# Performance work log

Hardware: AMD Instinct MI355X
Metric: run time of the kernel (lower is better)

Reference implementation:

```python
import jax, jax.numpy as jnp
import numpy as np

N_HEAD = 16
D_HEAD = 64
D_MODEL = 1024  # d_qry = d_key = d_val
D_HIDDEN = N_HEAD * D_HEAD


def setup_inputs() -> dict:
    key = jax.random.key(0)
    ks = jax.random.split(key, 9)
    b, n = 2, 2048
    s = 0.02
    return {
        "qry": jax.random.normal(ks[0], (b, n, D_MODEL), jnp.float32),
        "key": jax.random.normal(ks[1], (b, n, D_MODEL), jnp.float32),
        "val": jax.random.normal(ks[2], (b, n, D_MODEL), jnp.float32),
        "mask": jax.random.randint(ks[3], (b, n), 0, 2) > 0,  # key-side padding mask
        "Wq": jax.random.normal(ks[4], (D_MODEL, D_HIDDEN), jnp.float32) * s,
        "Wk": jax.random.normal(ks[5], (D_MODEL, D_HIDDEN), jnp.float32) * s,
        "Wv": jax.random.normal(ks[6], (D_MODEL, D_HIDDEN), jnp.float32) * s,
        "Wo": jax.random.normal(ks[7], (D_HIDDEN, D_MODEL), jnp.float32) * s,
        "bo": jax.random.normal(ks[8], (D_MODEL,), jnp.float32) * s,
    }


def reference(qry, key, val, mask, Wq, Wk, Wv, Wo, bo):
    b, n, _ = qry.shape
    scale = D_HEAD ** 0.5
    # projections, split into heads: [b, h, n, d]
    q = (qry @ Wq).reshape(b, n, N_HEAD, D_HEAD).transpose(0, 2, 1, 3)
    k = (key @ Wk).reshape(b, n, N_HEAD, D_HEAD).transpose(0, 2, 1, 3)
    v = (val @ Wv).reshape(b, n, N_HEAD, D_HEAD).transpose(0, 2, 1, 3)
    sim = jnp.einsum('bhid,bhjd->bhij', q, k) / scale  # full O(n^2) scores
    # key-side padding mask broadcast over heads and query positions
    sim = jnp.where(mask[:, None, None, :], sim, jnp.float32(-1e32))
    attn = jax.nn.softmax(sim, axis=-1)
    # NOTE: original applies dropout to `sim` after computing attn (a no-op on
    # the output); dropout=0.0 regardless, so attention weights are `attn`.
    x = jnp.einsum('bhij,bhjd->bhid', attn, v)
    x = x.transpose(0, 2, 1, 3).reshape(b, n, D_HIDDEN)
    return x @ Wo + bo
```

## Files before the change

### kernel.cpp

```cpp
#include <hip/hip_runtime.h>
#include <hip/hip_bf16.h>

using u16 = unsigned short;
using u32 = unsigned int;
using short8 = __attribute__((ext_vector_type(8))) short;
using f32x4  = __attribute__((ext_vector_type(4))) float;
using u32x4  = __attribute__((ext_vector_type(4))) u32;
using u32x2  = __attribute__((ext_vector_type(2))) u32;

union V16 { u32x4 u; short8 s; };

__device__ __forceinline__ u16 f2b(float f) {
  u32 u = __float_as_uint(f);
  u32 r = (u + 0x7FFFu + ((u >> 16) & 1u)) >> 16;
  return (u16)r;
}
__device__ __forceinline__ u32 pk2(u16 a, u16 b) {
  return (u32)a | ((u32)b << 16);
}
__device__ __forceinline__ u32 cvtpk(float lo, float hi) {
  u32 r;
  asm("v_cvt_pk_bf16_f32 %0, %1, %2" : "=v"(r) : "v"(lo), "v"(hi));
  return r;
}
__device__ __forceinline__ float ex2(float x) {
  float r;
  asm("v_exp_f32 %0, %1" : "=v"(r) : "v"(x));
  return r;
}
__device__ __forceinline__ void gld16(const u16* g, u16* l) {
  __builtin_amdgcn_global_load_lds(
      (const __attribute__((address_space(1))) u32*)g,
      (__attribute__((address_space(3))) u32*)l, 16, 0, 0);
}

#define KSCALE 0.18033688011f
#define SMAX   12.0f


__global__ __launch_bounds__(256) void wconv(
    const float* __restrict__ Wq, const float* __restrict__ Wk,
    const float* __restrict__ Wv, const float* __restrict__ Wo,
    u16* __restrict__ Wt, u16* __restrict__ WoT)
{
  __shared__ u16 T[64][130];
  const int zz = blockIdx.z;
  const float* src = (zz == 0) ? Wq : (zz == 1) ? Wk : (zz == 2) ? Wv : Wo;
  u16* dst = (zz < 3) ? (Wt + (size_t)zz * 1048576) : WoT;
  const int nt = blockIdx.x, ks = blockIdx.y;
  const int tid = threadIdx.x;

  {
    const int kl = tid >> 2, nl0 = (tid & 3) * 32;
    const float* sp = src + (size_t)(ks * 64 + kl) * 1024 + nt * 128 + nl0;
#pragma unroll
    for (int i = 0; i < 8; ++i) {
      f32x4 x = *(const f32x4*)(sp + i * 4);
      T[kl][nl0 + i * 4 + 0] = f2b(x[0]);
      T[kl][nl0 + i * 4 + 1] = f2b(x[1]);
      T[kl][nl0 + i * 4 + 2] = f2b(x[2]);
      T[kl][nl0 + i * 4 + 3] = f2b(x[3]);
    }
  }
  __syncthreads();

  const int c = tid >> 4, l0 = (tid & 15) * 4;
  u16* dp = dst + ((size_t)(nt * 16 + ks) * 16 + c) * 512 + l0 * 8;
#pragma unroll
  for (int dl = 0; dl < 4; ++dl) {
    const int l = l0 + dl;
    const int kl = (c & 1) * 32 + (l >> 4) * 8;
    const int nl = (c >> 3) * 64 + ((c >> 1) & 3) * 16 + (l & 15);
    u32x4 u;
#pragma unroll
    for (int p = 0; p < 4; ++p)
      u[p] = pk2(T[kl + 2 * p][nl], T[kl + 2 * p + 1][nl]);
    *(u32x4*)(dp + dl * 8) = u;
  }
}

__global__ __launch_bounds__(256) void maskscan(
    const int* __restrict__ mask, int* __restrict__ inv,
    float* __restrict__ cbias, int* __restrict__ ntb,
    u16* __restrict__ Kimg, u16* __restrict__ Vimg)
{
  const int h = blockIdx.x, b = blockIdx.y;
  const int tid = threadIdx.x;
  __shared__ int ssum[256];

  int m8[8], s = 0;
#pragma unroll
  for (int i = 0; i < 8; ++i) {
    m8[i] = mask[b * 2048 + tid * 8 + i] ? 1 : 0;
    s += m8[i];
  }
  ssum[tid] = s;
  __syncthreads();
  for (int off = 1; off < 256; off <<= 1) {
    int v = (tid >= off) ? ssum[tid - off] : 0;
    __syncthreads();
    ssum[tid] += v;
    __syncthreads();
  }
  const int nvalid = ssum[255];
  int run = ssum[tid] - s;

  if (h == 0) {
    int run2 = run;
#pragma unroll
    for (int i = 0; i < 8; ++i) {
      if (m8[i]) { inv[b * 2048 + run2] = tid * 8 + i; ++run2; }
    }
#pragma unroll
    for (int i = 0; i < 8; ++i) {
      const int idx = tid * 8 + i;
      cbias[b * 2048 + idx] = (idx < nvalid) ? -SMAX : -1e30f;
    }
    if (tid == 0) { ntb[b] = (nvalid + 63) >> 6; ntb[2 + b] = nvalid; }
  }

  const int pend = ((nvalid + 63) >> 6) << 6;
  for (int p = nvalid + tid; p < pend; p += 256) {
    const int kt2 = p >> 6, r = p & 63;
    const size_t base = ((size_t)((b * 16 + h) * 32 + kt2)) * 4096;
    const int t2 = ((r >> 5) << 1) | ((r >> 2) & 1);
    const int ll2 = (((r >> 3) & 3) << 2) | (r & 3);
#pragma unroll
    for (int s2 = 0; s2 < 2; ++s2)
#pragma unroll
      for (int lgk = 0; lgk < 4; ++lgk)
#pragma unroll
        for (int e = 0; e < 8; ++e)
          Kimg[base + (t2 * 2 + s2) * 512 + (lgk * 16 + ll2) * 8 + e] = 0;
    const int sv = r >> 5, lgv = (r >> 3) & 3, e0 = r & 7;
#pragma unroll
    for (int td = 0; td < 4; ++td)
#pragma unroll
      for (int llv = 0; llv < 16; ++llv)
        Vimg[base + (sv * 4 + td) * 512 + (lgv * 16 + llv) * 8 + e0] = 0;
  }
}

__global__ __launch_bounds__(256) void aconv(
    const float* __restrict__ Aq, const float* __restrict__ Ak,
    const float* __restrict__ Av, u16* __restrict__ Af,
    const int* __restrict__ inv, const int* __restrict__ ntbv,
    int z0, size_t zstride)
{
  const int z = blockIdx.z + z0;
  const float* A = (z == 0) ? Aq : (z == 1) ? Ak : Av;
  u16* dst = Af + (size_t)blockIdx.z * zstride;
  const int ks = blockIdx.x, mt = blockIdx.y;
  const int tid = threadIdx.x;
  const int r = tid >> 1, h = tid & 1;

  int srow = mt * 128 + r;
  if (z >= 1) {
    const int b = srow >> 11, cpos = srow & 2047;
    if (cpos >= ntbv[2 + b]) return;
    srow = b * 2048 + inv[b * 2048 + cpos];
  }

  const f32x4* sp = (const f32x4*)(A + (size_t)srow * 1024 + ks * 64 + h * 32);
  const int c = ((r >> 6) << 3) | (((r >> 4) & 3) << 1) | h;
  u16* dp = dst + ((size_t)(mt * 16 + ks) * 16 + c) * 512 + (r & 15) * 8;

#pragma unroll
  for (int lg = 0; lg < 4; ++lg) {
    f32x4 x0 = sp[2 * lg], x1 = sp[2 * lg + 1];
    u32x4 u;
    u[0] = cvtpk(x0[0], x0[1]); u[1] = cvtpk(x0[2], x0[3]);
    u[2] = cvtpk(x1[0], x1[1]); u[3] = cvtpk(x1[2], x1[3]);
    *(u32x4*)(dp + lg * 128) = u;
  }
}

__global__ __launch_bounds__(512, 4) void gemm_qkv_k(
    const u16* __restrict__ Af, const u16* __restrict__ Wt,
    u16* __restrict__ Qw, u16* __restrict__ Kw, u16* __restrict__ Vw,
    const int* __restrict__ ntbv, int z0, size_t azs)
{
  __shared__ u16 As[2][8192];
  __shared__ u16 Bs[2][8192];

  const int L = blockIdx.x;
  const int xcd = L & 7, idx = L >> 3;
  const int zi = idx >> 5;
  const int z = z0 + zi;
  const int mt = (z == 0) ? ((xcd << 2) | (idx & 3))
                          : (((idx & 3) << 3) | xcd);
  const int nt = (idx >> 2) & 7;

  if (z >= 1) {
    const int b0 = (mt * 128) >> 11;
    if ((mt * 128 & 2047) >= ntbv[2 + b0]) return;
  }

  const u16* Aimg = Af + (size_t)zi * azs;
  const u16* Bimg = Wt + (size_t)z * 1048576;
  u16* O = (z == 0) ? Qw : (z == 1) ? Kw : Vw;

  const int tid = threadIdx.x;
  const int w = tid >> 6, l = tid & 63, lg = l >> 4, ll = l & 15;
  const int wr = w >> 2, wc = w & 3;
  const size_t ab = (size_t)mt * 131072;
  const size_t bb = (size_t)nt * 131072;

  f32x4 acc[4][2];
#pragma unroll
  for (int i = 0; i < 4; ++i)
#pragma unroll
    for (int t = 0; t < 2; ++t)
      acc[i][t] = (f32x4){0.f, 0.f, 0.f, 0.f};

#define QKV_ISSUE(ksx, buf) do {                                           \
    const size_t ao_ = ab + (size_t)(ksx) * 8192;                          \
    const size_t bo_ = bb + (size_t)(ksx) * 8192;                          \
    gld16(Aimg + ao_ + (size_t)w * 512 + l * 8,       &As[buf][w * 512]);  \
    gld16(Aimg + ao_ + (size_t)(w + 8) * 512 + l * 8, &As[buf][(w + 8) * 512]); \
    gld16(Bimg + bo_ + (size_t)w * 512 + l * 8,       &Bs[buf][w * 512]);  \
    gld16(Bimg + bo_ + (size_t)(w + 8) * 512 + l * 8, &Bs[buf][(w + 8) * 512]); \
  } while (0)

  QKV_ISSUE(0, 0);

  for (int ks = 0; ks < 16; ++ks) {
    const int cur = ks & 1;
    asm volatile("s_waitcnt vmcnt(0)" ::: "memory");
    __builtin_amdgcn_sched_barrier(0);
    __builtin_amdgcn_s_barrier();
    __builtin_amdgcn_sched_barrier(0);

    if (ks + 1 < 16) QKV_ISSUE(ks + 1, cur ^ 1);

    short8 afr[2][4], bfr[2][2];
#pragma unroll
    for (int kk = 0; kk < 2; ++kk) {
#pragma unroll
      for (int i = 0; i < 4; ++i) {
        V16 v; v.u = *(const u32x4*)&As[cur][(wr * 8 + i * 2 + kk) * 512 + l * 8];
        afr[kk][i] = v.s;
      }
#pragma unroll
      for (int t = 0; t < 2; ++t) {
        V16 v; v.u = *(const u32x4*)&Bs[cur][((wc >> 1) * 8 + ((wc & 1) * 2 + t) * 2 + kk) * 512 + l * 8];
        bfr[kk][t] = v.s;
      }
    }
#pragma unroll
    for (int kk = 0; kk < 2; ++kk)
#pragma unroll
      for (int i = 0; i < 4; ++i)
#pragma unroll
        for (int t = 0; t < 2; ++t)
          acc[i][t] = __builtin_amdgcn_mfma_f32_16x16x32_bf16(afr[kk][i], bfr[kk][t], acc[i][t], 0, 0, 0);
  }
#undef QKV_ISSUE

  const int m0 = mt * 128, n0 = nt * 128;
  if (z == 0) {
#pragma unroll
    for (int i = 0; i < 4; ++i)
#pragma unroll
      for (int t = 0; t < 2; ++t) {
        const int n = n0 + wc * 32 + t * 16 + ll;
        const int h = n >> 6, dd = n & 63;
#pragma unroll
        for (int j = 0; j < 4; ++j) {
          const int m = m0 + wr * 64 + i * 16 + lg * 4 + j;
          const int bbk = m >> 11, pos = m & 2047;
          O[((size_t)(bbk * 16 + h) * 2048 + pos) * 64 + dd] = f2b(acc[i][t][j]);
        }
      }
  } else if (z == 1) {
    const int bbk = m0 >> 11;
    const int nv = ntbv[2 + bbk];
#pragma unroll
    for (int i = 0; i < 4; ++i)
#pragma unroll
      for (int t = 0; t < 2; ++t) {
        const int n = n0 + wc * 32 + t * 16 + ll;
        const int h = n >> 6, dd = n & 63;
        const int s = dd >> 5, lgk = (dd >> 3) & 3, e = dd & 7;
#pragma unroll
        for (int j = 0; j < 4; ++j) {
          const int m = m0 + wr * 64 + i * 16 + lg * 4 + j;
          const int cpos = m & 2047;
          if (cpos < nv) {
            const int kt2 = cpos >> 6, r = cpos & 63;
            const int t2 = ((r >> 5) << 1) | ((r >> 2) & 1);
            const int ll2 = (((r >> 3) & 3) << 2) | (r & 3);
            O[((size_t)((bbk * 16 + h) * 32 + kt2)) * 4096 + (t2 * 2 + s) * 512 + (lgk * 16 + ll2) * 8 + e]
                = f2b(acc[i][t][j] * KSCALE);
          }
        }
      }
  } else {
    const int bbk = m0 >> 11;
    const int nv = ntbv[2 + bbk];
#pragma unroll
    for (int i = 0; i < 4; ++i)
#pragma unroll
      for (int t = 0; t < 2; ++t) {
        const int n = n0 + wc * 32 + t * 16 + ll;
        const int h = n >> 6, dd = n & 63;
        const int td = dd >> 4, llv = dd & 15;
        const int mb0 = m0 + wr * 64 + i * 16 + lg * 4;
        const int cp0 = mb0 & 2047;
        const int kt2 = cp0 >> 6, kk = cp0 & 63;
        const int s = kk >> 5, lgv = (kk >> 3) & 3, e0 = kk & 7;
        u16* dstp = &O[((size_t)((bbk * 16 + h) * 32 + kt2)) * 4096 + (s * 4 + td) * 512 + (lgv * 16 + llv) * 8 + e0];
        if (cp0 + 3 < nv) {
          u32x2 wv;
          wv[0] = pk2(f2b(acc[i][t][0]), f2b(acc[i][t][1]));
          wv[1] = pk2(f2b(acc[i][t][2]), f2b(acc[i][t][3]));
          *(u32x2*)dstp = wv;
        } else {
#pragma unroll
          for (int j = 0; j < 4; ++j)
            if (cp0 + j < nv) dstp[j] = f2b(acc[i][t][j]);
        }
      }
  }
}

__global__ __launch_bounds__(256) void attn_k(
    const u16* __restrict__ Q, const u16* __restrict__ Kt, const u16* __restrict__ Vt,
    const float* __restrict__ cbias, const int* __restrict__ ntb,
    u16* __restrict__ Xf)
{
  __shared__ u16 Ls[2][8192];

  const int tid = threadIdx.x;
  const int w = tid >> 6, l = tid & 63, lg = l >> 4, ll = l & 15;
  const int qb = blockIdx.x, h = blockIdx.y, b = blockIdx.z;
  const size_t qbase = (size_t)(b * 16 + h) * 2048 * 64;
  const size_t tbase = (size_t)((b * 16 + h) * 32) * 4096;
  const int q0 = qb * 128 + w * 32;
  const int ntiles = ntb[b];

  short8 aq[2][2];
#pragma unroll
  for (int g = 0; g < 2; ++g)
#pragma unroll
    for (int s = 0; s < 2; ++s) {
      V16 v; v.u = *(const u32x4*)&Q[qbase + (size_t)(q0 + g * 16 + ll) * 64 + s * 32 + lg * 8];
      aq[g][s] = v.s;
    }

  float lrow[2] = {0.f, 0.f};
  f32x4 o[2][4];
#pragma unroll
  for (int g = 0; g < 2; ++g)
#pragma unroll
    for (int td = 0; td < 4; ++td) o[g][td] = (f32x4){0.f, 0.f, 0.f, 0.f};

  u32x4 rg[4];
#pragma unroll
  for (int q = 0; q < 4; ++q) {
    const int c = w * 4 + q;
    const u16* src = (c < 8) ? Kt : Vt;
    rg[q] = *(const u32x4*)&src[tbase + (c & 7) * 512 + l * 8];
  }
#pragma unroll
  for (int q = 0; q < 4; ++q)
    *(u32x4*)&Ls[0][(w * 4 + q) * 512 + l * 8] = rg[q];
  if (ntiles > 1) {
#pragma unroll
    for (int q = 0; q < 4; ++q) {
      const int c = w * 4 + q;
      const u16* src = (c < 8) ? Kt : Vt;
      rg[q] = *(const u32x4*)&src[tbase + 4096 + (c & 7) * 512 + l * 8];
    }
  }
  asm volatile("s_waitcnt lgkmcnt(0)" ::: "memory");
  __builtin_amdgcn_sched_barrier(0);
  __builtin_amdgcn_s_barrier();
  __builtin_amdgcn_sched_barrier(0);

  for (int kt = 0; kt < ntiles; ++kt) {
    const int cur = kt & 1;
    const int j0 = kt * 64;
    const u16* Lc = Ls[cur];

    f32x4 sc[2][4];
    __builtin_amdgcn_s_setprio(1);
#pragma unroll
    for (int t = 0; t < 4; ++t) {
      short8 bk0, bk1;
      { V16 v; v.u = *(const u32x4*)&Lc[(t * 2 + 0) * 512 + l * 8]; bk0 = v.s; }
      { V16 v; v.u = *(const u32x4*)&Lc[(t * 2 + 1) * 512 + l * 8]; bk1 = v.s; }
      f32x4 a0 = (f32x4){0.f, 0.f, 0.f, 0.f};
      f32x4 a1 = (f32x4){0.f, 0.f, 0.f, 0.f};
      a0 = __builtin_amdgcn_mfma_f32_16x16x32_bf16(bk0, aq[0][0], a0, 0, 0, 0);
      a1 = __builtin_amdgcn_mfma_f32_16x16x32_bf16(bk0, aq[1][0], a1, 0, 0, 0);
      a0 = __builtin_amdgcn_mfma_f32_16x16x32_bf16(bk1, aq[0][1], a0, 0, 0, 0);
      a1 = __builtin_amdgcn_mfma_f32_16x16x32_bf16(bk1, aq[1][1], a1, 0, 0, 0);
      const f32x4 cb = *(const f32x4*)&cbias[b * 2048 + j0 + ((t >> 1) << 5) + ((t & 1) << 2) + (lg << 3)];
#pragma unroll
      for (int j = 0; j < 4; ++j) {
        sc[0][t][j] = a0[j] + cb[j];
        sc[1][t][j] = a1[j] + cb[j];
      }
    }
    __builtin_amdgcn_s_setprio(0);

#pragma unroll
    for (int g = 0; g < 2; ++g) {
      f32x4 s4 = (f32x4){0.f, 0.f, 0.f, 0.f};
#pragma unroll
      for (int t = 0; t < 4; ++t)
#pragma unroll
        for (int j = 0; j < 4; ++j) {
          sc[g][t][j] = ex2(sc[g][t][j]);
          s4[j] += sc[g][t][j];
        }
      float rs = (s4[0] + s4[1]) + (s4[2] + s4[3]);
      rs += __shfl_xor(rs, 16);
      rs += __shfl_xor(rs, 32);
      lrow[g] += rs;
    }

    __builtin_amdgcn_s_setprio(1);
#pragma unroll
    for (int s = 0; s < 2; ++s) {
      V16 pb0, pb1;
      pb0.u[0] = cvtpk(sc[0][2 * s][0], sc[0][2 * s][1]);
      pb0.u[1] = cvtpk(sc[0][2 * s][2], sc[0][2 * s][3]);
      pb0.u[2] = cvtpk(sc[0][2 * s + 1][0], sc[0][2 * s + 1][1]);
      pb0.u[3] = cvtpk(sc[0][2 * s + 1][2], sc[0][2 * s + 1][3]);
      pb1.u[0] = cvtpk(sc[1][2 * s][0], sc[1][2 * s][1]);
      pb1.u[1] = cvtpk(sc[1][2 * s][2], sc[1][2 * s][3]);
      pb1.u[2] = cvtpk(sc[1][2 * s + 1][0], sc[1][2 * s + 1][1]);
      pb1.u[3] = cvtpk(sc[1][2 * s + 1][2], sc[1][2 * s + 1][3]);
#pragma unroll
      for (int td = 0; td < 4; ++td) {
        V16 v; v.u = *(const u32x4*)&Lc[4096 + (s * 4 + td) * 512 + l * 8];
        o[0][td] = __builtin_amdgcn_mfma_f32_16x16x32_bf16(v.s, pb0.s, o[0][td], 0, 0, 0);
        o[1][td] = __builtin_amdgcn_mfma_f32_16x16x32_bf16(v.s, pb1.s, o[1][td], 0, 0, 0);
      }
    }
    __builtin_amdgcn_s_setprio(0);

    if (kt + 1 < ntiles) {
#pragma unroll
      for (int q = 0; q < 4; ++q)
        *(u32x4*)&Ls[cur ^ 1][(w * 4 + q) * 512 + l * 8] = rg[q];
    }
    if (kt + 2 < ntiles) {
#pragma unroll
      for (int q = 0; q < 4; ++q) {
        const int c = w * 4 + q;
        const u16* src = (c < 8) ? Kt : Vt;
        rg[q] = *(const u32x4*)&src[tbase + (size_t)(kt + 2) * 4096 + (c & 7) * 512 + l * 8];
      }
    }
    asm volatile("s_waitcnt lgkmcnt(0)" ::: "memory");
    __builtin_amdgcn_sched_barrier(0);
    __builtin_amdgcn_s_barrier();
    __builtin_amdgcn_sched_barrier(0);
  }

#pragma unroll
  for (int g = 0; g < 2; ++g) {
    const float inv2 = 1.f / lrow[g];
    const int m = b * 2048 + q0 + g * 16 + ll;
    const int mt = m >> 7, mr = m & 127;
    const int e0 = (lg & 1) * 4;
#pragma unroll
    for (int td = 0; td < 4; ++td) {
      const int c = ((mr >> 6) << 3) | (((mr >> 4) & 3) << 1) | (td >> 1);
      const int lA = (((td << 1) + (lg >> 1)) & 3) * 16 + (mr & 15);
      u32x2 wv;
      wv[0] = cvtpk(o[g][td][0] * inv2, o[g][td][1] * inv2);
      wv[1] = cvtpk(o[g][td][2] * inv2, o[g][td][3] * inv2);
      *(u32x2*)&Xf[((size_t)(mt * 16 + h) * 16 + c) * 512 + lA * 8 + e0] = wv;
    }
  }
}

__global__ __launch_bounds__(512, 4) void gemm_out_k(
    const u16* __restrict__ Xf, const u16* __restrict__ WoF,
    const float* __restrict__ bo, float* __restrict__ out)
{
  __shared__ u16 As[3][8192];
  __shared__ u16 Bs[3][8192];

  const int L = blockIdx.x;
  const int xcd = L & 7, idx = L >> 3;
  const int mt = (xcd << 2) | (idx & 3);
  const int nt = idx >> 2;

  const int tid = threadIdx.x;
  const int w = tid >> 6, l = tid & 63, lg = l >> 4, ll = l & 15;
  const int wr = w >> 2, wc = w & 3;
  const size_t ab = (size_t)mt * 131072;
  const size_t bb = (size_t)nt * 131072;

  f32x4 acc[4][2];
#pragma unroll
  for (int i = 0; i < 4; ++i)
#pragma unroll
    for (int t = 0; t < 2; ++t)
      acc[i][t] = (f32x4){0.f, 0.f, 0.f, 0.f};

#define OUT_ISSUE(ksx, buf) do {                                           \
    const size_t ao_ = ab + (size_t)(ksx) * 8192;                          \
    const size_t bo_ = bb + (size_t)(ksx) * 8192;                          \
    gld16(Xf + ao_ + (size_t)w * 512 + l * 8,        &As[buf][w * 512]);   \
    gld16(Xf + ao_ + (size_t)(w + 8) * 512 + l * 8,  &As[buf][(w + 8) * 512]); \
    gld16(WoF + bo_ + (size_t)w * 512 + l * 8,       &Bs[buf][w * 512]);   \
    gld16(WoF + bo_ + (size_t)(w + 8) * 512 + l * 8, &Bs[buf][(w + 8) * 512]); \
  } while (0)

  OUT_ISSUE(0, 0);
  OUT_ISSUE(1, 1);

  for (int ks = 0; ks < 16; ++ks) {
    const int cur = ks % 3;
    if (ks < 15) asm volatile("s_waitcnt vmcnt(4)" ::: "memory");
    else         asm volatile("s_waitcnt vmcnt(0)" ::: "memory");
    __builtin_amdgcn_sched_barrier(0);
    __builtin_amdgcn_s_barrier();
    __builtin_amdgcn_sched_barrier(0);

    if (ks + 2 < 16) OUT_ISSUE(ks + 2, (ks + 2) % 3);

    short8 afr[2][4], bfr[2][2];
#pragma unroll
    for (int kk = 0; kk < 2; ++kk) {
#pragma unroll
      for (int i = 0; i < 4; ++i) {
        V16 v; v.u = *(const u32x4*)&As[cur][(wr * 8 + i * 2 + kk) * 512 + l * 8];
        afr[kk][i] = v.s;
      }
#pragma unroll
      for (int t = 0; t < 2; ++t) {
        V16 v; v.u = *(const u32x4*)&Bs[cur][((wc >> 1) * 8 + ((wc & 1) * 2 + t) * 2 + kk) * 512 + l * 8];
        bfr[kk][t] = v.s;
      }
    }
#pragma unroll
    for (int kk = 0; kk < 2; ++kk)
#pragma unroll
      for (int i = 0; i < 4; ++i)
#pragma unroll
        for (int t = 0; t < 2; ++t)
          acc[i][t] = __builtin_amdgcn_mfma_f32_16x16x32_bf16(afr[kk][i], bfr[kk][t], acc[i][t], 0, 0, 0);
  }
#undef OUT_ISSUE

  const int m0 = mt * 128, n0 = nt * 128;
#pragma unroll
  for (int i = 0; i < 4; ++i)
#pragma unroll
    for (int t = 0; t < 2; ++t) {
      const int n = n0 + wc * 32 + t * 16 + ll;
      const float bv = bo[n];
#pragma unroll
      for (int j = 0; j < 4; ++j) {
        const int m = m0 + wr * 64 + i * 16 + lg * 4 + j;
        out[(size_t)m * 1024 + n] = acc[i][t][j] + bv;
      }
    }
}

extern "C" void kernel_launch(void* const* d_in, const int* in_sizes, int n_in,
                              void* d_out, int out_size, void* d_ws, size_t ws_size,
                              hipStream_t stream) {
  const float* qry = (const float*)d_in[0];
  const float* key = (const float*)d_in[1];
  const float* val = (const float*)d_in[2];
  const int* mask  = (const int*)d_in[3];
  const float* Wq  = (const float*)d_in[4];
  const float* Wk  = (const float*)d_in[5];
  const float* Wv  = (const float*)d_in[6];
  const float* Wo  = (const float*)d_in[7];
  const float* bo  = (const float*)d_in[8];
  float* out = (float*)d_out;

  char* ws = (char*)d_ws;
  u16* Wt  = (u16*)(ws);
  u16* WoT = (u16*)(ws + 6291456);
  u16* Qw  = (u16*)(ws + 8388608);
  u16* Kw  = (u16*)(ws + 16777216);
  u16* Vw  = (u16*)(ws + 25165824);
  u16* Af  = (u16*)(ws + 33554432);
  u16* Xw  = (u16*)(ws + 33554432);

  int*   inv   = (int*)d_out;
  float* cbias = (float*)((char*)d_out + 16384);
  int*   ntb   = (int*)((char*)d_out + 32768);

  wconv<<<dim3(8, 16, 4), 256, 0, stream>>>(Wq, Wk, Wv, Wo, Wt, WoT);
  maskscan<<<dim3(16, 2), 256, 0, stream>>>(mask, inv, cbias, ntb, Kw, Vw);

  const bool big = (ws_size >= 58720256ull);
  if (big) {
    aconv<<<dim3(16, 32, 3), 256, 0, stream>>>(qry, key, val, Af, inv, ntb, 0, 4194304);
    gemm_qkv_k<<<dim3(768, 1, 1), 512, 0, stream>>>(Af, Wt, Qw, Kw, Vw, ntb, 0, 4194304);
  } else {
    for (int z = 0; z < 3; ++z) {
      aconv<<<dim3(16, 32, 1), 256, 0, stream>>>(qry, key, val, Af, inv, ntb, z, 0);
      gemm_qkv_k<<<dim3(256, 1, 1), 512, 0, stream>>>(Af, Wt, Qw, Kw, Vw, ntb, z, 0);
    }
  }
  attn_k<<<dim3(16, 16, 2), 256, 0, stream>>>(Qw, Kw, Vw, cbias, ntb, Xw);
  gemm_out_k<<<dim3(256, 1, 1), 512, 0, stream>>>(Xw, WoT, bo, out);
}
```

Measured before the change: 102.1 us.

## Triple-buffer QKV GEMM with half-K stages and two-deep prefetch

```diff
diff --git a/kernel.cpp b/kernel.cpp
--- a/kernel.cpp
+++ b/kernel.cpp
@@ -180,8 +180,8 @@
     u16* __restrict__ Qw, u16* __restrict__ Kw, u16* __restrict__ Vw,
     const int* __restrict__ ntbv, int z0, size_t azs)
 {
-  __shared__ u16 As[2][8192];
-  __shared__ u16 Bs[2][8192];
+  __shared__ u16 As[3][4096];
+  __shared__ u16 Bs[3][4096];
 
   const int L = blockIdx.x;
   const int xcd = L & 7, idx = L >> 3;
@@ -213,47 +213,43 @@
     for (int t = 0; t < 2; ++t)
       acc[i][t] = (f32x4){0.f, 0.f, 0.f, 0.f};
 
-#define QKV_ISSUE(ksx, buf) do {                                           \
-    const size_t ao_ = ab + (size_t)(ksx) * 8192;                          \
-    const size_t bo_ = bb + (size_t)(ksx) * 8192;                          \
-    gld16(Aimg + ao_ + (size_t)w * 512 + l * 8,       &As[buf][w * 512]);  \
-    gld16(Aimg + ao_ + (size_t)(w + 8) * 512 + l * 8, &As[buf][(w + 8) * 512]); \
-    gld16(Bimg + bo_ + (size_t)w * 512 + l * 8,       &Bs[buf][w * 512]);  \
-    gld16(Bimg + bo_ + (size_t)(w + 8) * 512 + l * 8, &Bs[buf][(w + 8) * 512]); \
+#define QKV_ISSUE(sx, bf) do {                                              \
+    const int ksi_ = (sx) >> 1, kkx_ = (sx) & 1;                            \
+    const size_t off_ = (size_t)ksi_ * 8192 +                               \
+        (size_t)(((w >> 2) * 8) + ((w & 3) * 2) + kkx_) * 512 + l * 8;      \
+    gld16(Aimg + ab + off_, &As[bf][w * 512]);                              \
+    gld16(Bimg + bb + off_, &Bs[bf][w * 512]);                              \
   } while (0)
 
   QKV_ISSUE(0, 0);
-
-  for (int ks = 0; ks < 16; ++ks) {
-    const int cur = ks & 1;
-    asm volatile("s_waitcnt vmcnt(0)" ::: "memory");
+  QKV_ISSUE(1, 1);
+
+  for (int s = 0; s < 32; ++s) {
+    const int cur = s % 3;
+    if (s < 31) asm volatile("s_waitcnt vmcnt(2)" ::: "memory");
+    else        asm volatile("s_waitcnt vmcnt(0)" ::: "memory");
     __builtin_amdgcn_sched_barrier(0);
     __builtin_amdgcn_s_barrier();
     __builtin_amdgcn_sched_barrier(0);
 
-    if (ks + 1 < 16) QKV_ISSUE(ks + 1, cur ^ 1);
-
-    short8 afr[2][4], bfr[2][2];
-#pragma unroll
-    for (int kk = 0; kk < 2; ++kk) {
-#pragma unroll
-      for (int i = 0; i < 4; ++i) {
-        V16 v; v.u = *(const u32x4*)&As[cur][(wr * 8 + i * 2 + kk) * 512 + l * 8];
-        afr[kk][i] = v.s;
-      }
-#pragma unroll
-      for (int t = 0; t < 2; ++t) {
-        V16 v; v.u = *(const u32x4*)&Bs[cur][((wc >> 1) * 8 + ((wc & 1) * 2 + t) * 2 + kk) * 512 + l * 8];
-        bfr[kk][t] = v.s;
-      }
-    }
-#pragma unroll
-    for (int kk = 0; kk < 2; ++kk)
-#pragma unroll
-      for (int i = 0; i < 4; ++i)
-#pragma unroll
-        for (int t = 0; t < 2; ++t)
-          acc[i][t] = __builtin_amdgcn_mfma_f32_16x16x32_bf16(afr[kk][i], bfr[kk][t], acc[i][t], 0, 0, 0);
+    if (s + 2 < 32) QKV_ISSUE(s + 2, (s + 2) % 3);
+
+    short8 afr[4], bfr[2];
+#pragma unroll
+    for (int i = 0; i < 4; ++i) {
+      V16 v; v.u = *(const u32x4*)&As[cur][(wr * 4 + i) * 512 + l * 8];
+      afr[i] = v.s;
+    }
+#pragma unroll
+    for (int t = 0; t < 2; ++t) {
+      V16 v; v.u = *(const u32x4*)&Bs[cur][((wc >> 1) * 4 + (wc & 1) * 2 + t) * 512 + l * 8];
+      bfr[t] = v.s;
+    }
+#pragma unroll
+    for (int i = 0; i < 4; ++i)
+#pragma unroll
+      for (int t = 0; t < 2; ++t)
+        acc[i][t] = __builtin_amdgcn_mfma_f32_16x16x32_bf16(afr[i], bfr[t], acc[i][t], 0, 0, 0);
   }
 #undef QKV_ISSUE
 
```

New measurement: 97.92 us (median of 2 runs). -4.1%, faster.
